# Optimization experiments

Measured on AMD Instinct MI355X. Metric: run time of the kernel, lower is better.

Reference implementation:

```python
import jax, jax.numpy as jnp
import numpy as np

N_NODES = 10000
N_EDGES = 320000


def gcn_conv(x, edge_index, edge_weight, W, b):
    """PyG GCNConv (add_self_loops=True, normalize=True) with edge weights.
    x: [N, Fin], edge_index: [2, E] (row=source, col=target), W: [Fin, Fout].
    """
    n = x.shape[0]
    row, col = edge_index[0], edge_index[1]
    # add self-loops with weight 1
    loop = jnp.arange(n, dtype=edge_index.dtype)
    row = jnp.concatenate([row, loop])
    col = jnp.concatenate([col, loop])
    ew = jnp.concatenate([edge_weight, jnp.ones((n,), dtype=edge_weight.dtype)])
    # symmetric normalization: D^-1/2 A D^-1/2
    deg = jax.ops.segment_sum(ew, col, num_segments=n)
    dinv = jnp.where(deg > 0, jax.lax.rsqrt(deg), 0.0)
    norm = dinv[row] * ew * dinv[col]  # [E+N]
    # linear transform first (smaller of the two widths often), then aggregate
    xw = x @ W  # [N, Fout]
    msg = norm[:, None] * xw[row]  # [E+N, Fout] gather
    out = jax.ops.segment_sum(msg, col, num_segments=n)  # scatter-add
    return out + b


def setup_inputs() -> dict:
    key = jax.random.key(0)
    ks = jax.random.split(key, 8)
    F = 256
    x = jax.random.normal(ks[0], (N_NODES, F), dtype=jnp.float32)
    edge_index = jax.random.randint(ks[1], (2, N_EDGES), 0, N_NODES, dtype=jnp.int64)
    edge_weights = jax.random.uniform(ks[2], (N_EDGES,), dtype=jnp.float32)
    s1 = 1.0 / np.sqrt(F)
    s2 = 1.0 / np.sqrt(2 * F)
    s3 = 1.0 / np.sqrt(3 * F)
    W1 = jax.random.normal(ks[3], (F, 2 * F), dtype=jnp.float32) * s1
    b1 = jnp.zeros((2 * F,), dtype=jnp.float32)
    W2 = jax.random.normal(ks[4], (2 * F, 3 * F), dtype=jnp.float32) * s2
    b2 = jnp.zeros((3 * F,), dtype=jnp.float32)
    W3 = jax.random.normal(ks[5], (3 * F, 8), dtype=jnp.float32) * s3
    b3 = jnp.zeros((8,), dtype=jnp.float32)
    return {"x": x, "edge_index": edge_index, "edge_weights": edge_weights,
            "W1": W1, "b1": b1, "W2": W2, "b2": b2, "W3": W3, "b3": b3}


def reference(x, edge_index, edge_weights, W1, b1, W2, b2, W3, b3):
    h = jax.nn.relu(gcn_conv(x, edge_index, edge_weights, W1, b1))
    h = jax.nn.relu(gcn_conv(h, edge_index, edge_weights, W2, b2))
    return gcn_conv(h, edge_index, edge_weights, W3, b3)
```

## Files before the change

kernel.cpp:

```cpp
#include <hip/hip_runtime.h>

#define N_NODES 10000
#define N_EDGES 320000
#define E_PAD (N_EDGES + 8 * N_NODES)

__device__ __forceinline__ unsigned short f2h_bits(float v) {
    _Float16 h = (_Float16)v;
    unsigned short u;
    __builtin_memcpy(&u, &h, 2);
    return u;
}
__device__ __forceinline__ float h2f_lo(unsigned int g) {
    unsigned short u = (unsigned short)(g & 0xFFFFu);
    _Float16 h; __builtin_memcpy(&h, &u, 2);
    return (float)h;
}
__device__ __forceinline__ float h2f_hi(unsigned int g) {
    unsigned short u = (unsigned short)(g >> 16);
    _Float16 h; __builtin_memcpy(&h, &u, 2);
    return (float)h;
}

__global__ __launch_bounds__(256) void setup_kernel(
        float* __restrict__ deg, int* __restrict__ counts,
        int* __restrict__ csr_src, float* __restrict__ csr_w,
        const float* __restrict__ x, unsigned short* __restrict__ xh,
        const float* __restrict__ W1, unsigned short* __restrict__ w1t,
        const float* __restrict__ W2, unsigned short* __restrict__ w2t) {
    int i = blockIdx.x * 256 + threadIdx.x;
    const int S0 = N_NODES;
    const int S1 = S0 + E_PAD;
    const int S2 = S1 + N_NODES * 256;
    const int S3 = S2 + 256 * 512;
    const int S4 = S3 + 512 * 768;
    if (i < S0) {
        deg[i] = 1.0f; counts[i] = 0;
    } else if (i < S1) {
        int j = i - S0;
        csr_src[j] = 0; csr_w[j] = 0.f;
    } else if (i < S2) {
        int j = i - S1;
        xh[j] = f2h_bits(x[j]);
    } else if (i < S3) {
        int j = i - S2;
        int k = j >> 9, n = j & 511;
        w1t[n * 256 + k] = f2h_bits(W1[j]);
    } else if (i < S4) {
        int j = i - S3;
        int k = j / 768, n = j - k * 768;
        w2t[n * 512 + k] = f2h_bits(W2[j]);
    }
}

__global__ __launch_bounds__(256) void count_slot_kernel(const int* __restrict__ col,
                                                         const float* __restrict__ ew,
                                                         float* __restrict__ deg,
                                                         int* __restrict__ counts,
                                                         int* __restrict__ slot, int e) {
    int i = blockIdx.x * 256 + threadIdx.x;
    if (i < e) {
        int c = col[i];
        slot[i] = atomicAdd(counts + c, 1);
        atomicAdd(deg + c, ew[i]);
    }
}

__global__ __launch_bounds__(1024) void scan_dinv_kernel(const int* __restrict__ counts,
                                                         int* __restrict__ ptr,
                                                         const float* __restrict__ deg,
                                                         float* __restrict__ dinv, int n) {
    __shared__ int wsum[16];
    __shared__ int woff[16];
    const int t = (int)threadIdx.x;
    const int lane = t & 63;
    const int wid = t >> 6;
    const int base = t * 10;
    int loc[10];
    int tot = 0;
#pragma unroll
    for (int q = 0; q < 10; ++q) {
        int i = base + q;
        int v = 0;
        if (i < n) {
            v = (counts[i] + 7) & ~7;
            float d = deg[i];
            dinv[i] = (d > 0.0f) ? rsqrtf(d) : 0.0f;
        }
        loc[q] = tot;
        tot += v;
    }
    int x = tot;
#pragma unroll
    for (int off = 1; off < 64; off <<= 1) {
        int u = __shfl_up(x, off);
        if (lane >= off) x += u;
    }
    if (lane == 63) wsum[wid] = x;
    __syncthreads();
    if (wid == 0 && lane < 16) {
        int s = wsum[lane];
        int y = s;
#pragma unroll
        for (int off = 1; off < 16; off <<= 1) {
            int u = __shfl_up(y, off);
            if (lane >= off) y += u;
        }
        woff[lane] = y - s;
        if (lane == 15) ptr[n] = y;
    }
    __syncthreads();
    const int tbase = woff[wid] + (x - tot);
#pragma unroll
    for (int q = 0; q < 10; ++q) {
        int i = base + q;
        if (i < n) ptr[i] = tbase + loc[q];
    }
}

__global__ __launch_bounds__(256) void scatter_kernel(const int* __restrict__ row,
                                                      const int* __restrict__ col,
                                                      const float* __restrict__ ew,
                                                      const float* __restrict__ dinv,
                                                      const int* __restrict__ ptr,
                                                      const int* __restrict__ slot,
                                                      int* __restrict__ csr_src,
                                                      float* __restrict__ csr_w, int e) {
    int i = blockIdx.x * 256 + threadIdx.x;
    if (i < e) {
        int c = col[i], r = row[i];
        int pos = ptr[c] + slot[i];
        csr_src[pos] = r;
        csr_w[pos] = dinv[r] * ew[i] * dinv[c];
    }
}

template <int F, int SSHIFT>
__global__ __launch_bounds__(256) void agg_slice_kernel(const unsigned int* __restrict__ xpk,
                                                        const int* __restrict__ ptr,
                                                        const int* __restrict__ csr_src,
                                                        const float* __restrict__ csr_w,
                                                        const float* __restrict__ dinv,
                                                        unsigned int* __restrict__ o) {
    constexpr int F2 = F / 2;
    const int b = (int)blockIdx.x;
    const int slice = b & ((1 << SSHIFT) - 1);
    const int node = __builtin_amdgcn_readfirstlane(
        (b >> SSHIFT) * 4 + ((int)threadIdx.x >> 6));
    const int lane = (int)threadIdx.x & 63;
    const int f2 = slice * 64 + lane;
    const float di = dinv[node];
    const float si = di * di;
    unsigned int gs = xpk[node * F2 + f2];
    float acc0 = si * h2f_lo(gs);
    float acc1 = si * h2f_hi(gs);
    const int s = ptr[node], e = ptr[node + 1];

    for (int j = s; j < e; j += 8) {
        int4   sa = *(const int4*)(csr_src + j);
        int4   sb = *(const int4*)(csr_src + j + 4);
        float4 wa = *(const float4*)(csr_w + j);
        float4 wb = *(const float4*)(csr_w + j + 4);
        unsigned int g0 = xpk[sa.x * F2 + f2];
        unsigned int g1 = xpk[sa.y * F2 + f2];
        unsigned int g2 = xpk[sa.z * F2 + f2];
        unsigned int g3 = xpk[sa.w * F2 + f2];
        unsigned int g4 = xpk[sb.x * F2 + f2];
        unsigned int g5 = xpk[sb.y * F2 + f2];
        unsigned int g6 = xpk[sb.z * F2 + f2];
        unsigned int g7 = xpk[sb.w * F2 + f2];
        acc0 += wa.x * h2f_lo(g0) + wa.y * h2f_lo(g1) + wa.z * h2f_lo(g2) + wa.w * h2f_lo(g3);
        acc1 += wa.x * h2f_hi(g0) + wa.y * h2f_hi(g1) + wa.z * h2f_hi(g2) + wa.w * h2f_hi(g3);
        acc0 += wb.x * h2f_lo(g4) + wb.y * h2f_lo(g5) + wb.z * h2f_lo(g6) + wb.w * h2f_lo(g7);
        acc1 += wb.x * h2f_hi(g4) + wb.y * h2f_hi(g5) + wb.z * h2f_hi(g6) + wb.w * h2f_hi(g7);
    }

    unsigned short h0 = f2h_bits(acc0);
    unsigned short h1 = f2h_bits(acc1);
    o[node * F2 + f2] = ((unsigned int)h1 << 16) | h0;
}

typedef _Float16 half8 __attribute__((ext_vector_type(8)));
typedef float f32x4 __attribute__((ext_vector_type(4)));

#define TM 128
#define TN 128
#define BK 32
#define LDS_A 0
#define LDS_B 8192
#define LDS_BUF 16384

__device__ __forceinline__ void async16(const unsigned short* g, unsigned char* l) {
    __builtin_amdgcn_global_load_lds(
        (const __attribute__((address_space(1))) unsigned int*)g,
        (__attribute__((address_space(3))) unsigned int*)l, 16, 0, 0);
}

__global__ __launch_bounds__(256, 3) void gemm_mfma_kernel(
        const unsigned short* __restrict__ A,
        const unsigned short* __restrict__ Bt,
        const float* __restrict__ bias,
        unsigned short* __restrict__ Cb,
        int M, int K, int N) {
    __shared__ unsigned char lds[2 * LDS_BUF];
    const int t = (int)threadIdx.x;

    const int gx = (int)gridDim.x;
    const int nwg = gx * (int)gridDim.y;
    const int lin = (int)blockIdx.y * gx + (int)blockIdx.x;
    const int xcd = lin & 7, idx = lin >> 3;
    const int q = nwg >> 3, r = nwg & 7;
    const int logi = (xcd < r ? xcd * (q + 1) : r * (q + 1) + (xcd - r) * q) + idx;
    const int bm = (logi / gx) * TM;
    const int bn = (logi % gx) * TN;

    const int lane = t & 63;
    const int wave = t >> 6;
    const int wm = (wave & 1) * 64;
    const int wn = (wave >> 1) * 64;

    const int slr = lane >> 2;
    const int scc = (lane & 3) ^ ((slr >> 1) & 3);
    const int bi0 = wave * 2, bi1 = wave * 2 + 1;
    const unsigned short* gA0 = A + (size_t)(bm + bi0 * 16 + slr) * K + scc * 8;
    const unsigned short* gA1 = A + (size_t)(bm + bi1 * 16 + slr) * K + scc * 8;
    const unsigned short* gB0 = Bt + (size_t)(bn + bi0 * 16 + slr) * K + scc * 8;
    const unsigned short* gB1 = Bt + (size_t)(bn + bi1 * 16 + slr) * K + scc * 8;

    const int quad = lane >> 4;
    const int lr16 = lane & 15;
    const int fs = (quad ^ ((lr16 >> 1) & 3)) * 16;

    f32x4 acc[4][4];
    const f32x4 zero4 = {0.f, 0.f, 0.f, 0.f};
#pragma unroll
    for (int i = 0; i < 4; ++i)
#pragma unroll
        for (int j = 0; j < 4; ++j) acc[i][j] = zero4;

    const int KT = K / BK;

    auto stage = [&](int kt, int buf) {
        const int k0 = kt * BK;
        unsigned char* b = &lds[buf * LDS_BUF];
        async16(gA0 + k0, b + LDS_A + bi0 * 1024);
        async16(gA1 + k0, b + LDS_A + bi1 * 1024);
        async16(gB0 + k0, b + LDS_B + bi0 * 1024);
        async16(gB1 + k0, b + LDS_B + bi1 * 1024);
    };

    stage(0, 0);
    __syncthreads();

    for (int kt = 0; kt < KT; ++kt) {
        const int buf = kt & 1;
        if (kt + 1 < KT) stage(kt + 1, buf ^ 1);

        unsigned char* b = &lds[buf * LDS_BUF];
        half8 av[4], bv[4];
#pragma unroll
        for (int i = 0; i < 4; ++i) {
            int ro = (wm + i * 16 + lr16) * 64 + fs;
            av[i] = *(const half8*)(b + LDS_A + ro);
        }
#pragma unroll
        for (int j = 0; j < 4; ++j) {
            int ro = (wn + j * 16 + lr16) * 64 + fs;
            bv[j] = *(const half8*)(b + LDS_B + ro);
        }
#pragma unroll
        for (int i = 0; i < 4; ++i)
#pragma unroll
            for (int j = 0; j < 4; ++j)
                acc[i][j] = __builtin_amdgcn_mfma_f32_16x16x32_f16(av[i], bv[j], acc[i][j], 0, 0, 0);
        __syncthreads();
    }

    float bcol[4];
#pragma unroll
    for (int j = 0; j < 4; ++j) bcol[j] = bias[bn + wn + j * 16 + lr16];
#pragma unroll
    for (int i = 0; i < 4; ++i) {
#pragma unroll
        for (int r2 = 0; r2 < 4; ++r2) {
            int m = bm + wm + i * 16 + quad * 4 + r2;
            if (m < M) {
#pragma unroll
                for (int j = 0; j < 4; ++j) {
                    float vv = fmaxf(acc[i][j][r2] + bcol[j], 0.f);
                    Cb[(size_t)m * N + bn + wn + j * 16 + lr16] = f2h_bits(vv);
                }
            }
        }
    }
}

__global__ __launch_bounds__(64) void gemm_n8_kernel(const unsigned int* __restrict__ Apk,
                                                     const float* __restrict__ B,
                                                     float* __restrict__ C) {
    const int m = blockIdx.x;
    const int lane = (int)threadIdx.x;
    const unsigned int* a = Apk + m * 384;
    float acc[8] = {};
#pragma unroll
    for (int it = 0; it < 6; ++it) {
        int j2 = lane + it * 64;
        unsigned int av = a[j2];
        float a0 = h2f_lo(av), a1 = h2f_hi(av);
        const float* B0 = B + (size_t)(2 * j2) * 8;
        float4 p0 = *(const float4*)(B0);
        float4 p1 = *(const float4*)(B0 + 4);
        float4 q0 = *(const float4*)(B0 + 8);
        float4 q1 = *(const float4*)(B0 + 12);
        acc[0] += a0 * p0.x + a1 * q0.x; acc[1] += a0 * p0.y + a1 * q0.y;
        acc[2] += a0 * p0.z + a1 * q0.z; acc[3] += a0 * p0.w + a1 * q0.w;
        acc[4] += a0 * p1.x + a1 * q1.x; acc[5] += a0 * p1.y + a1 * q1.y;
        acc[6] += a0 * p1.z + a1 * q1.z; acc[7] += a0 * p1.w + a1 * q1.w;
    }
#pragma unroll
    for (int off = 32; off > 0; off >>= 1) {
#pragma unroll
        for (int i = 0; i < 8; ++i) acc[i] += __shfl_down(acc[i], off);
    }
    if (lane == 0) {
#pragma unroll
        for (int i = 0; i < 8; ++i) C[(size_t)m * 8 + i] = acc[i];
    }
}

__global__ __launch_bounds__(64) void agg8_kernel(const float* __restrict__ xw,
                                                  const int* __restrict__ ptr,
                                                  const int* __restrict__ csr_src,
                                                  const float* __restrict__ csr_w,
                                                  const float* __restrict__ dinv,
                                                  const float* __restrict__ bias,
                                                  float* __restrict__ out) {
    int node = blockIdx.x;
    int lane = threadIdx.x;
    float acc[8] = {};
    int s = ptr[node], e = ptr[node + 1];
    for (int j = s + lane; j < e; j += 64) {
        int src = csr_src[j];
        float w = csr_w[j];
        float4 g0 = *(const float4*)(xw + (size_t)src * 8);
        float4 g1 = *(const float4*)(xw + (size_t)src * 8 + 4);
        acc[0] += w * g0.x; acc[1] += w * g0.y; acc[2] += w * g0.z; acc[3] += w * g0.w;
        acc[4] += w * g1.x; acc[5] += w * g1.y; acc[6] += w * g1.z; acc[7] += w * g1.w;
    }
#pragma unroll
    for (int off = 32; off > 0; off >>= 1) {
#pragma unroll
        for (int i = 0; i < 8; ++i) acc[i] += __shfl_down(acc[i], off);
    }
    if (lane == 0) {
        float di = dinv[node];
        float si = di * di;
#pragma unroll
        for (int i = 0; i < 8; ++i)
            out[(size_t)node * 8 + i] = acc[i] + si * xw[(size_t)node * 8 + i] + bias[i];
    }
}


extern "C" void kernel_launch(void* const* d_in, const int* in_sizes, int n_in,
                              void* d_out, int out_size, void* d_ws, size_t ws_size,
                              hipStream_t stream) {
    const int N = N_NODES, E = N_EDGES;
    const int N_PAD = ((N + TM - 1) / TM) * TM;
    const float* x   = (const float*)d_in[0];
    const int*   ei  = (const int*)d_in[1];
    const float* ew  = (const float*)d_in[2];
    const float* W1  = (const float*)d_in[3];
    const float* b1  = (const float*)d_in[4];
    const float* W2  = (const float*)d_in[5];
    const float* b2  = (const float*)d_in[6];
    const float* W3  = (const float*)d_in[7];
    const float* b3  = (const float*)d_in[8];
    float* out = (float*)d_out;

    const int* row = ei;
    const int* col = ei + E;

    char* ws = (char*)d_ws;
    size_t off = 0;
    auto alloc = [&](size_t bytes) {
        void* p = ws + off;
        off += (bytes + 255) & ~(size_t)255;
        return p;
    };
    float*          deg     = (float*)alloc((size_t)N * 4);
    float*          dinv    = (float*)alloc((size_t)N * 4);
    int*            counts  = (int*)alloc((size_t)N * 4);
    int*            col_ptr = (int*)alloc((size_t)(N + 1) * 4);
    int*            slot    = (int*)alloc((size_t)E * 4);
    int*            csr_src = (int*)alloc((size_t)E_PAD * 4);
    float*          csr_w   = (float*)alloc((size_t)E_PAD * 4);
    unsigned short* xh      = (unsigned short*)alloc((size_t)N * 256 * 2);
    unsigned short* h1h     = (unsigned short*)alloc((size_t)N * 512 * 2);
    unsigned short* h2h     = (unsigned short*)alloc((size_t)N * 768 * 2);
    unsigned short* Aagg    = (unsigned short*)alloc((size_t)N_PAD * 512 * 2);
    unsigned short* W1t     = (unsigned short*)alloc((size_t)512 * 256 * 2);
    unsigned short* W2t     = (unsigned short*)alloc((size_t)768 * 512 * 2);
    float*          xw8     = (float*)alloc((size_t)N * 8 * 4);
    (void)ws_size;

    int nb_edges = (E + 255) / 256;

    {
        int tot = N + E_PAD + N * 256 + 256 * 512 + 512 * 768;
        setup_kernel<<<(tot + 255) / 256, 256, 0, stream>>>(
            deg, counts, csr_src, csr_w, x, xh, W1, W1t, W2, W2t);
    }
    count_slot_kernel<<<nb_edges, 256, 0, stream>>>(col, ew, deg, counts, slot, E);
    scan_dinv_kernel<<<1, 1024, 0, stream>>>(counts, col_ptr, deg, dinv, N);
    scatter_kernel<<<nb_edges, 256, 0, stream>>>(row, col, ew, dinv, col_ptr, slot,
                                                 csr_src, csr_w, E);

    agg_slice_kernel<256, 1><<<N * 2 / 4, 256, 0, stream>>>(
        (const unsigned int*)xh, col_ptr, csr_src, csr_w, dinv, (unsigned int*)Aagg);
    {
        dim3 grid(512 / TN, N_PAD / TM);
        gemm_mfma_kernel<<<grid, 256, 0, stream>>>(Aagg, W1t, b1, h1h, N, 256, 512);
    }
    agg_slice_kernel<512, 2><<<N * 4 / 4, 256, 0, stream>>>(
        (const unsigned int*)h1h, col_ptr, csr_src, csr_w, dinv, (unsigned int*)Aagg);
    {
        dim3 grid(768 / TN, N_PAD / TM);
        gemm_mfma_kernel<<<grid, 256, 0, stream>>>(Aagg, W2t, b2, h2h, N, 512, 768);
    }
    gemm_n8_kernel<<<N, 64, 0, stream>>>((const unsigned int*)h2h, W3, xw8);
    agg8_kernel<<<N, 64, 0, stream>>>(xw8, col_ptr, csr_src, csr_w, dinv, b3, out);

    (void)out_size; (void)n_in; (void)in_sizes;
}
```

Before: 229.8 us.

## Fuse layer-3 W3 projection into layer-2 GEMM epilogue with atomic accumulation

The layer-2 MFMA GEMM epilogue now multiplies its ReLU outputs by W3 directly, reduces across the 16 lanes by shuffles, and atomically adds partial 8-wide results into xw8. This removes the h2 fp16 intermediate write/read and the separate gemm_n8 launch. xw8 is zeroed inside the layer-2 aggregation kernel so no extra launch is needed. The cost is 6 column blocks times atomics per row, plus non-deterministic float summation order and h2 no longer rounded to fp16 before the projection.

```diff
diff --git a/kernel.cpp b/kernel.cpp
--- a/kernel.cpp
+++ b/kernel.cpp
@@ -140,7 +140,13 @@
                                                         const int* __restrict__ csr_src,
                                                         const float* __restrict__ csr_w,
                                                         const float* __restrict__ dinv,
-                                                        unsigned int* __restrict__ o) {
+                                                        unsigned int* __restrict__ o,
+                                                        float* __restrict__ zbuf,
+                                                        int zcount) {
+    if (zbuf) {
+        int g = (int)blockIdx.x * 256 + (int)threadIdx.x;
+        if (g < zcount) zbuf[g] = 0.f;
+    }
     constexpr int F2 = F / 2;
     const int b = (int)blockIdx.x;
     const int slice = b & ((1 << SSHIFT) - 1);
@@ -195,11 +201,14 @@
         (__attribute__((address_space(3))) unsigned int*)l, 16, 0, 0);
 }
 
+template <bool FUSE_W3>
 __global__ __launch_bounds__(256, 3) void gemm_mfma_kernel(
         const unsigned short* __restrict__ A,
         const unsigned short* __restrict__ Bt,
         const float* __restrict__ bias,
         unsigned short* __restrict__ Cb,
+        const float* __restrict__ W3,
+        float* __restrict__ xw8,
         int M, int K, int N) {
     __shared__ unsigned char lds[2 * LDS_BUF];
     const int t = (int)threadIdx.x;
@@ -278,52 +287,61 @@
     float bcol[4];
 #pragma unroll
     for (int j = 0; j < 4; ++j) bcol[j] = bias[bn + wn + j * 16 + lr16];
-#pragma unroll
-    for (int i = 0; i < 4; ++i) {
-#pragma unroll
-        for (int r2 = 0; r2 < 4; ++r2) {
-            int m = bm + wm + i * 16 + quad * 4 + r2;
-            if (m < M) {
+
+    if constexpr (!FUSE_W3) {
+#pragma unroll
+        for (int i = 0; i < 4; ++i) {
+#pragma unroll
+            for (int r2 = 0; r2 < 4; ++r2) {
+                int m = bm + wm + i * 16 + quad * 4 + r2;
+                if (m < M) {
+#pragma unroll
+                    for (int j = 0; j < 4; ++j) {
+                        float vv = fmaxf(acc[i][j][r2] + bcol[j], 0.f);
+                        Cb[(size_t)m * N + bn + wn + j * 16 + lr16] = f2h_bits(vv);
+                    }
+                }
+            }
+        }
+    } else {
+        float4 w3a[4], w3b[4];
+#pragma unroll
+        for (int j = 0; j < 4; ++j) {
+            const float* wr = W3 + (size_t)(bn + wn + j * 16 + lr16) * 8;
+            w3a[j] = *(const float4*)wr;
+            w3b[j] = *(const float4*)(wr + 4);
+        }
+#pragma unroll
+        for (int i = 0; i < 4; ++i) {
+#pragma unroll
+            for (int r2 = 0; r2 < 4; ++r2) {
+                int m = bm + wm + i * 16 + quad * 4 + r2;
+                float s0 = 0.f, s1 = 0.f, s2 = 0.f, s3 = 0.f;
+                float s4 = 0.f, s5 = 0.f, s6 = 0.f, s7 = 0.f;
 #pragma unroll
                 for (int j = 0; j < 4; ++j) {
                     float vv = fmaxf(acc[i][j][r2] + bcol[j], 0.f);
-                    Cb[(size_t)m * N + bn + wn + j * 16 + lr16] = f2h_bits(vv);
+                    s0 += vv * w3a[j].x; s1 += vv * w3a[j].y;
+                    s2 += vv * w3a[j].z; s3 += vv * w3a[j].w;
+                    s4 += vv * w3b[j].x; s5 += vv * w3b[j].y;
+                    s6 += vv * w3b[j].z; s7 += vv * w3b[j].w;
+                }
+#pragma unroll
+                for (int mk = 1; mk < 16; mk <<= 1) {
+                    s0 += __shfl_xor(s0, mk); s1 += __shfl_xor(s1, mk);
+                    s2 += __shfl_xor(s2, mk); s3 += __shfl_xor(s3, mk);
+                    s4 += __shfl_xor(s4, mk); s5 += __shfl_xor(s5, mk);
+                    s6 += __shfl_xor(s6, mk); s7 += __shfl_xor(s7, mk);
+                }
+                if (lr16 == 0 && m < M) {
+                    float* xp = xw8 + (size_t)m * 8;
+                    atomicAdd(xp + 0, s0); atomicAdd(xp + 1, s1);
+                    atomicAdd(xp + 2, s2); atomicAdd(xp + 3, s3);
+                    atomicAdd(xp + 4, s4); atomicAdd(xp + 5, s5);
+                    atomicAdd(xp + 6, s6); atomicAdd(xp + 7, s7);
                 }
             }
         }
-    }
-}
-
-__global__ __launch_bounds__(64) void gemm_n8_kernel(const unsigned int* __restrict__ Apk,
-                                                     const float* __restrict__ B,
-                                                     float* __restrict__ C) {
-    const int m = blockIdx.x;
-    const int lane = (int)threadIdx.x;
-    const unsigned int* a = Apk + m * 384;
-    float acc[8] = {};
-#pragma unroll
-    for (int it = 0; it < 6; ++it) {
-        int j2 = lane + it * 64;
-        unsigned int av = a[j2];
-        float a0 = h2f_lo(av), a1 = h2f_hi(av);
-        const float* B0 = B + (size_t)(2 * j2) * 8;
-        float4 p0 = *(const float4*)(B0);
-        float4 p1 = *(const float4*)(B0 + 4);
-        float4 q0 = *(const float4*)(B0 + 8);
-        float4 q1 = *(const float4*)(B0 + 12);
-        acc[0] += a0 * p0.x + a1 * q0.x; acc[1] += a0 * p0.y + a1 * q0.y;
-        acc[2] += a0 * p0.z + a1 * q0.z; acc[3] += a0 * p0.w + a1 * q0.w;
-        acc[4] += a0 * p1.x + a1 * q1.x; acc[5] += a0 * p1.y + a1 * q1.y;
-        acc[6] += a0 * p1.z + a1 * q1.z; acc[7] += a0 * p1.w + a1 * q1.w;
-    }
-#pragma unroll
-    for (int off = 32; off > 0; off >>= 1) {
-#pragma unroll
-        for (int i = 0; i < 8; ++i) acc[i] += __shfl_down(acc[i], off);
-    }
-    if (lane == 0) {
-#pragma unroll
-        for (int i = 0; i < 8; ++i) C[(size_t)m * 8 + i] = acc[i];
     }
 }
 
@@ -396,7 +414,6 @@
     float*          csr_w   = (float*)alloc((size_t)E_PAD * 4);
     unsigned short* xh      = (unsigned short*)alloc((size_t)N * 256 * 2);
     unsigned short* h1h     = (unsigned short*)alloc((size_t)N * 512 * 2);
-    unsigned short* h2h     = (unsigned short*)alloc((size_t)N * 768 * 2);
     unsigned short* Aagg    = (unsigned short*)alloc((size_t)N_PAD * 512 * 2);
     unsigned short* W1t     = (unsigned short*)alloc((size_t)512 * 256 * 2);
     unsigned short* W2t     = (unsigned short*)alloc((size_t)768 * 512 * 2);
@@ -416,18 +433,21 @@
                                                  csr_src, csr_w, E);
 
     agg_slice_kernel<256, 1><<<N * 2 / 4, 256, 0, stream>>>(
-        (const unsigned int*)xh, col_ptr, csr_src, csr_w, dinv, (unsigned int*)Aagg);
+        (const unsigned int*)xh, col_ptr, csr_src, csr_w, dinv,
+        (unsigned int*)Aagg, nullptr, 0);
     {
         dim3 grid(512 / TN, N_PAD / TM);
-        gemm_mfma_kernel<<<grid, 256, 0, stream>>>(Aagg, W1t, b1, h1h, N, 256, 512);
+        gemm_mfma_kernel<false><<<grid, 256, 0, stream>>>(
+            Aagg, W1t, b1, h1h, nullptr, nullptr, N, 256, 512);
     }
     agg_slice_kernel<512, 2><<<N * 4 / 4, 256, 0, stream>>>(
-        (const unsigned int*)h1h, col_ptr, csr_src, csr_w, dinv, (unsigned int*)Aagg);
+        (const unsigned int*)h1h, col_ptr, csr_src, csr_w, dinv,
+        (unsigned int*)Aagg, xw8, N * 8);
     {
         dim3 grid(768 / TN, N_PAD / TM);
-        gemm_mfma_kernel<<<grid, 256, 0, stream>>>(Aagg, W2t, b2, h2h, N, 512, 768);
-    }
-    gemm_n8_kernel<<<N, 64, 0, stream>>>((const unsigned int*)h2h, W3, xw8);
+        gemm_mfma_kernel<true><<<grid, 256, 0, stream>>>(
+            Aagg, W2t, b2, nullptr, W3, xw8, N, 512, 768);
+    }
     agg8_kernel<<<N, 64, 0, stream>>>(xw8, col_ptr, csr_src, csr_w, dinv, b3, out);
 
     (void)out_size; (void)n_in; (void)in_sizes;
```

New measurement: 288.9 us. 25.7% more time.
